# Kernel tuning notes

Measured on AMD Instinct MI355X. Metric: run time of the kernel, lower is better.

The kernel has to match this reference:

```python
import jax, jax.numpy as jnp
import numpy as np

B, N, H = 2, 2048, 1024
NUM_HEADS = 16
HEAD_DIM = H // NUM_HEADS
SCALE = HEAD_DIM ** -0.5


def setup_inputs() -> dict:
    key = jax.random.key(0)
    k1, k2, k3, k4 = jax.random.split(key, 4)
    s = 0.02
    return {
        "x": jax.random.normal(k1, (B, N, H), dtype=jnp.float32),
        "x2": jax.random.normal(k2, (B, N, H), dtype=jnp.float32),
        "Wqkv": jax.random.normal(k3, (H, 3 * H), dtype=jnp.float32) * s,
        "Wout": jax.random.normal(k4, (H, H), dtype=jnp.float32) * s,
        "bout": jnp.zeros((H,), dtype=jnp.float32),
    }


def _split_qkv(t):
    # t: [B, N, 3H] -> [3, B, h, N, d]
    b, n, _ = t.shape
    t = t.reshape(b, n, 3, NUM_HEADS, HEAD_DIM)
    return jnp.transpose(t, (2, 0, 3, 1, 4))


def reference(x, x2, Wqkv, Wout, bout):
    # shared qkv projection applied to both streams (bias=False)
    qkv2 = _split_qkv(x2 @ Wqkv)  # k, v from x2
    k, v = qkv2[1], qkv2[2]       # [B, h, N2, d]
    qkv1 = _split_qkv(x @ Wqkv)   # q from x
    q = qkv1[0]                   # [B, h, N, d]

    att = jax.nn.softmax(jnp.einsum("bhxd,bhyd->bhxy", q, k) * SCALE, axis=-1)
    out = jnp.einsum("bhxy,bhyd->bhxd", att, v)        # [B, h, N, d]
    out = jnp.transpose(out, (0, 2, 1, 3)).reshape(x.shape[0], x.shape[1], -1)
    return out @ Wout + bout
```

## Files before the change

kernel.cpp:

```cpp
#include <hip/hip_runtime.h>

#define B_ 2
#define N_ 2048
#define H_ 1024
#define NH_ 16
#define D_ 64

typedef _Float16 f16;
typedef _Float16 f16x2 __attribute__((ext_vector_type(2)));
typedef _Float16 f16x4 __attribute__((ext_vector_type(4)));
typedef _Float16 f16x8 __attribute__((ext_vector_type(8)));
typedef float f32x4 __attribute__((ext_vector_type(4)));

#define MFMA16(a, b, c) __builtin_amdgcn_mfma_f32_16x16x32_f16((a), (b), (c), 0, 0, 0)
#define MFMA16K(a, b, c) __builtin_amdgcn_mfma_f32_16x16x16f16((a), (b), (c), 0, 0, 0)

__device__ __forceinline__ void cp16(void* lds, const void* g) {
  __builtin_amdgcn_global_load_lds(
      (const __attribute__((address_space(1))) void*)g,
      (__attribute__((address_space(3))) void*)lds, 16, 0, 0);
}

__device__ __forceinline__ f16x4 pk4(float a, float b, float c, float d) {
  auto lo = __builtin_amdgcn_cvt_pkrtz(a, b);
  auto hi = __builtin_amdgcn_cvt_pkrtz(c, d);
  f16x4 r;
  r[0] = (f16)lo[0]; r[1] = (f16)lo[1]; r[2] = (f16)hi[0]; r[3] = (f16)hi[1];
  return r;
}

__global__ __launch_bounds__(256) void prep(
    const float* __restrict__ x, const float* __restrict__ x2,
    f16* __restrict__ xo, f16* __restrict__ x2o,
    const float* __restrict__ Wqkv, f16* __restrict__ WqkvT,
    const float* __restrict__ Wout, f16* __restrict__ WoutT) {
  const int bid = blockIdx.x;
  const int t = threadIdx.x;

  if (bid < 4096) {
    const float* __restrict__ src = (bid < 2048) ? x : x2;
    f16* __restrict__ dst = (bid < 2048) ? xo : x2o;
    const size_t i = ((size_t)(bid & 2047) * 256 + t) * 8;
    float4 v0 = ((const float4*)(src + i))[0];
    float4 v1 = ((const float4*)(src + i))[1];
    f16x8 o;
    o[0] = (f16)v0.x; o[1] = (f16)v0.y; o[2] = (f16)v0.z; o[3] = (f16)v0.w;
    o[4] = (f16)v1.x; o[5] = (f16)v1.y; o[6] = (f16)v1.z; o[7] = (f16)v1.w;
    *(f16x8*)(dst + i) = o;
    return;
  }

  const float* __restrict__ W;
  f16* __restrict__ Wt;
  int cb, kb, rows, ncols;
  if (bid < 4864) {
    int j = bid - 4096;
    W = Wqkv; Wt = WqkvT; rows = H_; ncols = 3 * H_;
    cb = (j % 48) * 64; kb = (j / 48) * 64;
  } else {
    int j = bid - 4864;
    W = Wout; Wt = WoutT; rows = H_; ncols = H_;
    cb = (j & 15) * 64; kb = (j >> 4) * 64;
  }

  __shared__ f16 T[64][72];
  {
    const int k = t >> 2, c0 = (t & 3) * 16;
    const float* wp = W + (size_t)(kb + k) * ncols + cb + c0;
    float4 w0 = ((const float4*)wp)[0];
    float4 w1 = ((const float4*)wp)[1];
    float4 w2 = ((const float4*)wp)[2];
    float4 w3 = ((const float4*)wp)[3];
    T[c0 + 0][k] = (f16)w0.x;  T[c0 + 1][k] = (f16)w0.y;
    T[c0 + 2][k] = (f16)w0.z;  T[c0 + 3][k] = (f16)w0.w;
    T[c0 + 4][k] = (f16)w1.x;  T[c0 + 5][k] = (f16)w1.y;
    T[c0 + 6][k] = (f16)w1.z;  T[c0 + 7][k] = (f16)w1.w;
    T[c0 + 8][k] = (f16)w2.x;  T[c0 + 9][k] = (f16)w2.y;
    T[c0 + 10][k] = (f16)w2.z; T[c0 + 11][k] = (f16)w2.w;
    T[c0 + 12][k] = (f16)w3.x; T[c0 + 13][k] = (f16)w3.y;
    T[c0 + 14][k] = (f16)w3.z; T[c0 + 15][k] = (f16)w3.w;
  }
  __syncthreads();
  {
    const int c = t >> 2, k0 = (t & 3) * 16;
    f16* op = Wt + (size_t)(cb + c) * rows + kb + k0;
    *(f16x8*)(op + 0) = *(const f16x8*)(&T[c][k0]);
    *(f16x8*)(op + 8) = *(const f16x8*)(&T[c][k0 + 8]);
  }
}

__global__ __launch_bounds__(256) void qkv_mfma(
    const f16* __restrict__ Xc, const f16* __restrict__ X2c,
    const f16* __restrict__ Wt, f16* __restrict__ Qo,
    f16* __restrict__ Ko, f16* __restrict__ Vto) {
  const int bid = blockIdx.x;
  const int rb = (bid & 31) * 128;
  const int cb = (bid >> 5) * 128;
  const int t = threadIdx.x;
  const int lane = t & 63, wid = t >> 6;
  const int quad = lane >> 4, n16 = lane & 15;
  const int wm = wid >> 1, wn = wid & 1;

  const f16* __restrict__ A = (cb < H_) ? Xc : X2c;
  const int seg = cb >> 10;
  const float qscale = (seg == 0) ? 0.125f * 1.44269504f : 1.0f;

  __shared__ f16 As[128 * 32];
  __shared__ f16 Bs[128 * 32];

  f32x4 acc[4][4];
#pragma unroll
  for (int i = 0; i < 4; ++i)
#pragma unroll
    for (int j = 0; j < 4; ++j) acc[i][j] = (f32x4){0.f, 0.f, 0.f, 0.f};

  int srow0 = wid * 16 + (lane >> 2);
  int srow1 = 64 + srow0;
  int gl0 = ((lane & 3) ^ ((srow0 >> 1) & 3)) * 8;
  int gl1 = ((lane & 3) ^ ((srow1 >> 1) & 3)) * 8;
  const f16* gA0 = A + (size_t)(rb + srow0) * H_ + gl0;
  const f16* gA1 = A + (size_t)(rb + srow1) * H_ + gl1;
  const f16* gB0 = Wt + (size_t)(cb + srow0) * H_ + gl0;
  const f16* gB1 = Wt + (size_t)(cb + srow1) * H_ + gl1;
  f16* lA0 = &As[wid * 512];
  f16* lA1 = &As[2048 + wid * 512];
  f16* lB0 = &Bs[wid * 512];
  f16* lB1 = &Bs[2048 + wid * 512];

  const int fsw = (quad ^ ((n16 >> 1) & 3)) * 8;
  int aoff[4], boff[4];
#pragma unroll
  for (int i = 0; i < 4; ++i) {
    aoff[i] = (wm * 64 + i * 16 + n16) * 32 + fsw;
    boff[i] = (wn * 64 + i * 16 + n16) * 32 + fsw;
  }

  const bool vseg = (seg == 2);
  for (int kt = 0; kt < H_; kt += 32) {
    __syncthreads();
    cp16(lA0, gA0); cp16(lA1, gA1);
    cp16(lB0, gB0); cp16(lB1, gB1);
    gA0 += 32; gA1 += 32; gB0 += 32; gB1 += 32;
    __syncthreads();

    f16x8 af[4], bf[4];
#pragma unroll
    for (int mt = 0; mt < 4; ++mt) af[mt] = *(const f16x8*)(&As[aoff[mt]]);
#pragma unroll
    for (int nt = 0; nt < 4; ++nt) bf[nt] = *(const f16x8*)(&Bs[boff[nt]]);
    if (!vseg) {
#pragma unroll
      for (int mt = 0; mt < 4; ++mt)
#pragma unroll
        for (int nt = 0; nt < 4; ++nt)
          acc[mt][nt] = MFMA16(af[mt], bf[nt], acc[mt][nt]);
    } else {
#pragma unroll
      for (int mt = 0; mt < 4; ++mt)
#pragma unroll
        for (int nt = 0; nt < 4; ++nt)
          acc[mt][nt] = MFMA16(bf[nt], af[mt], acc[mt][nt]);
    }
  }

  if (!vseg) {
    f16* __restrict__ outp = (seg == 0) ? Qo : Ko;
#pragma unroll
    for (int mt = 0; mt < 4; ++mt)
#pragma unroll
      for (int nt = 0; nt < 4; ++nt)
#pragma unroll
        for (int r = 0; r < 4; ++r) {
          int grow = rb + wm * 64 + mt * 16 + quad * 4 + r;
          int gcol = cb + wn * 64 + nt * 16 + n16;
          int bb = grow >> 11, nn = grow & 2047;
          int hh = (gcol >> 6) & 15, dd = gcol & 63;
          outp[(((size_t)(bb * NH_ + hh)) * N_ + nn) * D_ + dd] =
              (f16)(acc[mt][nt][r] * qscale);
        }
  } else {
#pragma unroll
    for (int mt = 0; mt < 4; ++mt)
#pragma unroll
      for (int nt = 0; nt < 4; ++nt)
#pragma unroll
        for (int r = 0; r < 4; ++r) {
          int gcol = cb + wn * 64 + nt * 16 + quad * 4 + r;
          int grow = rb + wm * 64 + mt * 16 + n16;
          int bb = grow >> 11, nn = grow & 2047;
          int hh = (gcol >> 6) & 15, dd = gcol & 63;
          Vto[(((size_t)(bb * NH_ + hh)) * D_ + dd) * N_ + nn] =
              (f16)acc[mt][nt][r];
        }
  }
}

__global__ __launch_bounds__(256) void attn5(
    const f16* __restrict__ Q, const f16* __restrict__ K,
    const f16* __restrict__ Vt, f16* __restrict__ AO) {
  const int bh = blockIdx.y;
  const int b = bh >> 4, h = bh & 15;
  const int qb = blockIdx.x * 64;
  const int t = threadIdx.x;
  const int lane = t & 63, wid = t >> 6;
  const int quad = lane >> 4, n16 = lane & 15;
  const int qh = wid & 1;
  const int kh = wid >> 1;

  const f16* __restrict__ Qp = Q + (size_t)bh * N_ * D_;
  const f16* __restrict__ Kp = K + (size_t)bh * N_ * D_;
  const f16* __restrict__ Vp = Vt + (size_t)bh * D_ * N_;

  __shared__ f16 Ks[2][64 * 64];
  __shared__ f16 Vs[2][64 * 64];

  f16x8 qf[2][2];
#pragma unroll
  for (int qc = 0; qc < 2; ++qc) {
    const f16* qp = Qp + (size_t)(qb + qh * 32 + qc * 16 + n16) * D_ + quad * 8;
    qf[qc][0] = *(const f16x8*)(qp);
    qf[qc][1] = *(const f16x8*)(qp + 32);
  }

  f32x4 o[2][4];
#pragma unroll
  for (int i = 0; i < 2; ++i)
#pragma unroll
    for (int j = 0; j < 4; ++j) o[i][j] = (f32x4){0.f, 0.f, 0.f, 0.f};
  f32x4 lacc[2];
  lacc[0] = (f32x4){0.f, 0.f, 0.f, 0.f};
  lacc[1] = (f32x4){0.f, 0.f, 0.f, 0.f};
  const f16x4 onesb = (f16x4){(f16)1.f, (f16)1.f, (f16)1.f, (f16)1.f};

  const int srow0 = wid * 8 + (lane >> 3);
  const int srow1 = 32 + srow0;
  const int gl0 = ((lane & 7) ^ (srow0 & 7)) * 8;
  const int gl1 = ((lane & 7) ^ (srow1 & 7)) * 8;
  const f16* gK0 = Kp + (size_t)srow0 * D_ + gl0;
  const f16* gK1 = Kp + (size_t)srow1 * D_ + gl1;
  const f16* gV0 = Vp + (size_t)srow0 * N_ + gl0;
  const f16* gV1 = Vp + (size_t)srow1 * N_ + gl1;

  const int fs0 = (quad ^ (n16 & 7)) * 8;
  const int fs1 = ((quad + 4) ^ (n16 & 7)) * 8;
  int voff[4];
#pragma unroll
  for (int kc = 0; kc < 4; ++kc)
    voff[kc] = n16 * 64 + (((kc * 2 + (quad >> 1)) ^ (n16 & 7)) * 8) + (quad & 1) * 4;

  const f16* __restrict__ ks = &Ks[kh][0];
  const f16* __restrict__ vs = &Vs[kh][0];

  for (int kt = 0; kt < N_; kt += 128) {
    __syncthreads();
    cp16(&Ks[0][wid * 512], gK0 + (size_t)kt * D_);
    cp16(&Ks[0][2048 + wid * 512], gK1 + (size_t)kt * D_);
    cp16(&Ks[1][wid * 512], gK0 + (size_t)(kt + 64) * D_);
    cp16(&Ks[1][2048 + wid * 512], gK1 + (size_t)(kt + 64) * D_);
    cp16(&Vs[0][wid * 512], gV0 + kt);
    cp16(&Vs[0][2048 + wid * 512], gV1 + kt);
    cp16(&Vs[1][wid * 512], gV0 + kt + 64);
    cp16(&Vs[1][2048 + wid * 512], gV1 + kt + 64);
    __syncthreads();

    f32x4 s[2][4];
#pragma unroll
    for (int kc = 0; kc < 4; ++kc) {
      const f16x8 kf0 = *(const f16x8*)(&ks[(kc * 16 + n16) * 64 + fs0]);
      const f16x8 kf1 = *(const f16x8*)(&ks[(kc * 16 + n16) * 64 + fs1]);
#pragma unroll
      for (int qc = 0; qc < 2; ++qc) {
        f32x4 sv = (f32x4){0.f, 0.f, 0.f, 0.f};
        sv = MFMA16(kf0, qf[qc][0], sv);
        sv = MFMA16(kf1, qf[qc][1], sv);
        s[qc][kc] = sv;
      }
    }

    f16x4 pa[2][4];
#pragma unroll
    for (int qc = 0; qc < 2; ++qc)
#pragma unroll
      for (int kc = 0; kc < 4; ++kc) {
        float p0 = __builtin_amdgcn_exp2f(s[qc][kc][0]);
        float p1 = __builtin_amdgcn_exp2f(s[qc][kc][1]);
        float p2 = __builtin_amdgcn_exp2f(s[qc][kc][2]);
        float p3 = __builtin_amdgcn_exp2f(s[qc][kc][3]);
        pa[qc][kc] = pk4(p0, p1, p2, p3);
      }
#pragma unroll
    for (int kc = 0; kc < 4; ++kc) {
      lacc[0] = MFMA16K(pa[0][kc], onesb, lacc[0]);
      lacc[1] = MFMA16K(pa[1][kc], onesb, lacc[1]);
    }

#pragma unroll
    for (int kc = 0; kc < 4; ++kc)
#pragma unroll
      for (int dt = 0; dt < 4; ++dt) {
        const f16x4 vb = *(const f16x4*)(&vs[dt * 1024 + voff[kc]]);
        o[0][dt] = MFMA16K(pa[0][kc], vb, o[0][dt]);
        o[1][dt] = MFMA16K(pa[1][kc], vb, o[1][dt]);
      }
  }

  __syncthreads();
  float* red = (float*)&Ks[0][0];
  if (kh == 1) {
    float* p = red + ((size_t)(qh * 64 + lane)) * 40;
#pragma unroll
    for (int qc = 0; qc < 2; ++qc) {
#pragma unroll
      for (int dt = 0; dt < 4; ++dt)
        *(f32x4*)(p + (qc * 4 + dt) * 4) = o[qc][dt];
      *(f32x4*)(p + 32 + qc * 4) = lacc[qc];
    }
  }
  __syncthreads();
  if (kh == 0) {
    const float* p = red + ((size_t)(qh * 64 + lane)) * 40;
#pragma unroll
    for (int qc = 0; qc < 2; ++qc) {
#pragma unroll
      for (int dt = 0; dt < 4; ++dt) {
        f32x4 v = *(const f32x4*)(p + (qc * 4 + dt) * 4);
#pragma unroll
        for (int r = 0; r < 4; ++r) o[qc][dt][r] += v[r];
      }
      f32x4 lv = *(const f32x4*)(p + 32 + qc * 4);
#pragma unroll
      for (int r = 0; r < 4; ++r) lacc[qc][r] += lv[r];
    }

#pragma unroll
    for (int qc = 0; qc < 2; ++qc)
#pragma unroll
      for (int r = 0; r < 4; ++r) {
        float inv = 1.0f / lacc[qc][r];
        int nrow = qb + qh * 32 + qc * 16 + quad * 4 + r;
        f16* aop = AO + ((size_t)(b * N_ + nrow)) * H_ + h * 64;
#pragma unroll
        for (int dt = 0; dt < 4; ++dt)
          aop[dt * 16 + n16] = (f16)(o[qc][dt][r] * inv);
      }
  }
}

__global__ __launch_bounds__(256) void out_mfma(
    const f16* __restrict__ A, const f16* __restrict__ Wt,
    const float* __restrict__ bias, float* __restrict__ out) {
  const int bid = blockIdx.x;
  const int rb = (bid & 31) * 128;
  const int cb = (bid >> 5) * 128;
  const int t = threadIdx.x;
  const int lane = t & 63, wid = t >> 6;
  const int quad = lane >> 4, n16 = lane & 15;
  const int wm = wid >> 1, wn = wid & 1;

  __shared__ f16 As[128 * 32];
  __shared__ f16 Bs[128 * 32];

  f32x4 acc[4][4];
#pragma unroll
  for (int i = 0; i < 4; ++i)
#pragma unroll
    for (int j = 0; j < 4; ++j) acc[i][j] = (f32x4){0.f, 0.f, 0.f, 0.f};

  int srow0 = wid * 16 + (lane >> 2);
  int srow1 = 64 + srow0;
  int gl0 = ((lane & 3) ^ ((srow0 >> 1) & 3)) * 8;
  int gl1 = ((lane & 3) ^ ((srow1 >> 1) & 3)) * 8;
  const f16* gA0 = A + (size_t)(rb + srow0) * H_ + gl0;
  const f16* gA1 = A + (size_t)(rb + srow1) * H_ + gl1;
  const f16* gB0 = Wt + (size_t)(cb + srow0) * H_ + gl0;
  const f16* gB1 = Wt + (size_t)(cb + srow1) * H_ + gl1;
  f16* lA0 = &As[wid * 512];
  f16* lA1 = &As[2048 + wid * 512];
  f16* lB0 = &Bs[wid * 512];
  f16* lB1 = &Bs[2048 + wid * 512];

  const int fsw = (quad ^ ((n16 >> 1) & 3)) * 8;
  int aoff[4], boff[4];
#pragma unroll
  for (int i = 0; i < 4; ++i) {
    aoff[i] = (wm * 64 + i * 16 + n16) * 32 + fsw;
    boff[i] = (wn * 64 + i * 16 + n16) * 32 + fsw;
  }

  for (int kt = 0; kt < H_; kt += 32) {
    __syncthreads();
    cp16(lA0, gA0); cp16(lA1, gA1);
    cp16(lB0, gB0); cp16(lB1, gB1);
    gA0 += 32; gA1 += 32; gB0 += 32; gB1 += 32;
    __syncthreads();

    f16x8 af[4], bf[4];
#pragma unroll
    for (int mt = 0; mt < 4; ++mt) af[mt] = *(const f16x8*)(&As[aoff[mt]]);
#pragma unroll
    for (int nt = 0; nt < 4; ++nt) bf[nt] = *(const f16x8*)(&Bs[boff[nt]]);
#pragma unroll
    for (int mt = 0; mt < 4; ++mt)
#pragma unroll
      for (int nt = 0; nt < 4; ++nt)
        acc[mt][nt] = MFMA16(af[mt], bf[nt], acc[mt][nt]);
  }

#pragma unroll
  for (int nt = 0; nt < 4; ++nt) {
    int gcol = cb + wn * 64 + nt * 16 + n16;
    float bv = bias[gcol];
#pragma unroll
    for (int mt = 0; mt < 4; ++mt)
#pragma unroll
      for (int r = 0; r < 4; ++r) {
        int grow = rb + wm * 64 + mt * 16 + quad * 4 + r;
        out[(size_t)grow * H_ + gcol] = acc[mt][nt][r] + bv;
      }
  }
}

extern "C" void kernel_launch(void* const* d_in, const int* in_sizes, int n_in,
                              void* d_out, int out_size, void* d_ws, size_t ws_size,
                              hipStream_t stream) {
  const float* x    = (const float*)d_in[0];
  const float* x2   = (const float*)d_in[1];
  const float* Wqkv = (const float*)d_in[2];
  const float* Wout = (const float*)d_in[3];
  const float* bout = (const float*)d_in[4];
  float* out = (float*)d_out;

  const size_t per = (size_t)B_ * NH_ * N_ * D_;
  f16* Xc    = (f16*)d_ws;
  f16* X2c   = Xc + per;
  f16* Qw    = X2c + per;
  f16* Kw    = Qw + per;
  f16* Vtw   = Kw + per;
  f16* AO    = Vtw + per;
  f16* WqkvT = AO + per;
  f16* WoutT = WqkvT + (size_t)3072 * 1024;

  prep<<<dim3(5120), 256, 0, stream>>>(x, x2, Xc, X2c, Wqkv, WqkvT, Wout, WoutT);
  qkv_mfma<<<dim3(768), 256, 0, stream>>>(Xc, X2c, WqkvT, Qw, Kw, Vtw);
  attn5<<<dim3(32, 32), 256, 0, stream>>>(Qw, Kw, Vtw, AO);
  out_mfma<<<dim3(256), 256, 0, stream>>>(AO, WoutT, bout, out);
}
```

Baseline: 214.3 us.

## Double-buffer K/V tiles and widen attention blocks to 128 query rows

The attention kernel now uses 512-thread blocks that each cover 128 query rows, so every K/V tile loaded into LDS serves twice as many queries. K/V loading is restructured into a two-stage ping-pong buffer: the next 128-key tile is issued with global-to-LDS copies while the current tile is being computed, with one barrier per iteration instead of two. This aims to hide global load latency and cut K/V traffic per query. In exchange it uses 64KB of LDS per block and launches half as many blocks, which may limit occupancy.

```diff
diff --git a/kernel.cpp b/kernel.cpp
--- a/kernel.cpp
+++ b/kernel.cpp
@@ -195,29 +195,28 @@
   }
 }
 
-__global__ __launch_bounds__(256) void attn5(
+__global__ __launch_bounds__(512) void attn6(
     const f16* __restrict__ Q, const f16* __restrict__ K,
     const f16* __restrict__ Vt, f16* __restrict__ AO) {
   const int bh = blockIdx.y;
   const int b = bh >> 4, h = bh & 15;
-  const int qb = blockIdx.x * 64;
+  const int qb = blockIdx.x * 128;
   const int t = threadIdx.x;
   const int lane = t & 63, wid = t >> 6;
   const int quad = lane >> 4, n16 = lane & 15;
-  const int qh = wid & 1;
-  const int kh = wid >> 1;
+  const int qg = wid >> 1;
+  const int kh = wid & 1;
 
   const f16* __restrict__ Qp = Q + (size_t)bh * N_ * D_;
   const f16* __restrict__ Kp = K + (size_t)bh * N_ * D_;
   const f16* __restrict__ Vp = Vt + (size_t)bh * D_ * N_;
 
-  __shared__ f16 Ks[2][64 * 64];
-  __shared__ f16 Vs[2][64 * 64];
+  __shared__ f16 smem[32768];
 
   f16x8 qf[2][2];
 #pragma unroll
   for (int qc = 0; qc < 2; ++qc) {
-    const f16* qp = Qp + (size_t)(qb + qh * 32 + qc * 16 + n16) * D_ + quad * 8;
+    const f16* qp = Qp + (size_t)(qb + qg * 32 + qc * 16 + n16) * D_ + quad * 8;
     qf[qc][0] = *(const f16x8*)(qp);
     qf[qc][1] = *(const f16x8*)(qp + 32);
   }
@@ -232,14 +231,10 @@
   lacc[1] = (f32x4){0.f, 0.f, 0.f, 0.f};
   const f16x4 onesb = (f16x4){(f16)1.f, (f16)1.f, (f16)1.f, (f16)1.f};
 
-  const int srow0 = wid * 8 + (lane >> 3);
-  const int srow1 = 32 + srow0;
-  const int gl0 = ((lane & 7) ^ (srow0 & 7)) * 8;
-  const int gl1 = ((lane & 7) ^ (srow1 & 7)) * 8;
-  const f16* gK0 = Kp + (size_t)srow0 * D_ + gl0;
-  const f16* gK1 = Kp + (size_t)srow1 * D_ + gl1;
-  const f16* gV0 = Vp + (size_t)srow0 * N_ + gl0;
-  const f16* gV1 = Vp + (size_t)srow1 * N_ + gl1;
+  const int srow = t >> 3;
+  const int sgl = ((t & 7) ^ (srow & 7)) * 8;
+  const f16* gK = Kp + (size_t)srow * D_ + sgl;
+  const f16* gV = Vp + (size_t)srow * N_ + sgl;
 
   const int fs0 = (quad ^ (n16 & 7)) * 8;
   const int fs1 = ((quad + 4) ^ (n16 & 7)) * 8;
@@ -248,20 +243,29 @@
   for (int kc = 0; kc < 4; ++kc)
     voff[kc] = n16 * 64 + (((kc * 2 + (quad >> 1)) ^ (n16 & 7)) * 8) + (quad & 1) * 4;
 
-  const f16* __restrict__ ks = &Ks[kh][0];
-  const f16* __restrict__ vs = &Vs[kh][0];
-
-  for (int kt = 0; kt < N_; kt += 128) {
+  {
+    f16* kb = smem;
+    f16* vb = smem + 16384;
+    cp16(kb + wid * 512, gK);
+    cp16(kb + 4096 + wid * 512, gK + (size_t)64 * D_);
+    cp16(vb + wid * 512, gV);
+    cp16(vb + 4096 + wid * 512, gV + 64);
+  }
+
+  for (int i = 0; i < 16; ++i) {
     __syncthreads();
-    cp16(&Ks[0][wid * 512], gK0 + (size_t)kt * D_);
-    cp16(&Ks[0][2048 + wid * 512], gK1 + (size_t)kt * D_);
-    cp16(&Ks[1][wid * 512], gK0 + (size_t)(kt + 64) * D_);
-    cp16(&Ks[1][2048 + wid * 512], gK1 + (size_t)(kt + 64) * D_);
-    cp16(&Vs[0][wid * 512], gV0 + kt);
-    cp16(&Vs[0][2048 + wid * 512], gV1 + kt);
-    cp16(&Vs[1][wid * 512], gV0 + kt + 64);
-    cp16(&Vs[1][2048 + wid * 512], gV1 + kt + 64);
-    __syncthreads();
+    if (i < 15) {
+      const int nk = (i + 1) * 128;
+      const int nb = (i + 1) & 1;
+      f16* kb = smem + nb * 8192;
+      f16* vb = smem + 16384 + nb * 8192;
+      cp16(kb + wid * 512, gK + (size_t)nk * D_);
+      cp16(kb + 4096 + wid * 512, gK + (size_t)(nk + 64) * D_);
+      cp16(vb + wid * 512, gV + nk);
+      cp16(vb + 4096 + wid * 512, gV + nk + 64);
+    }
+    const f16* ks = smem + (i & 1) * 8192 + kh * 4096;
+    const f16* vs = smem + 16384 + (i & 1) * 8192 + kh * 4096;
 
     f32x4 s[2][4];
 #pragma unroll
@@ -305,9 +309,9 @@
   }
 
   __syncthreads();
-  float* red = (float*)&Ks[0][0];
+  float* red = (float*)smem;
   if (kh == 1) {
-    float* p = red + ((size_t)(qh * 64 + lane)) * 40;
+    float* p = red + ((size_t)(qg * 64 + lane)) * 40;
 #pragma unroll
     for (int qc = 0; qc < 2; ++qc) {
 #pragma unroll
@@ -318,7 +322,7 @@
   }
   __syncthreads();
   if (kh == 0) {
-    const float* p = red + ((size_t)(qh * 64 + lane)) * 40;
+    const float* p = red + ((size_t)(qg * 64 + lane)) * 40;
 #pragma unroll
     for (int qc = 0; qc < 2; ++qc) {
 #pragma unroll
@@ -337,7 +341,7 @@
 #pragma unroll
       for (int r = 0; r < 4; ++r) {
         float inv = 1.0f / lacc[qc][r];
-        int nrow = qb + qh * 32 + qc * 16 + quad * 4 + r;
+        int nrow = qb + qg * 32 + qc * 16 + quad * 4 + r;
         f16* aop = AO + ((size_t)(b * N_ + nrow)) * H_ + h * 64;
 #pragma unroll
         for (int dt = 0; dt < 4; ++dt)
@@ -442,6 +446,6 @@
 
   prep<<<dim3(5120), 256, 0, stream>>>(x, x2, Xc, X2c, Wqkv, WqkvT, Wout, WoutT);
   qkv_mfma<<<dim3(768), 256, 0, stream>>>(Xc, X2c, WqkvT, Qw, Kw, Vtw);
-  attn5<<<dim3(32, 32), 256, 0, stream>>>(Qw, Kw, Vtw, AO);
+  attn6<<<dim3(16, 32), 512, 0, stream>>>(Qw, Kw, Vtw, AO);
   out_mfma<<<dim3(256), 256, 0, stream>>>(AO, WoutT, bout, out);
 }
```

After: 203.6 us. 1.05x faster.
